# Performance work log

Hardware: AMD Instinct MI355X
Metric: run time of the kernel (lower is better)

The kernel has to match this reference:

```python
import jax, jax.numpy as jnp
import numpy as np


def setup_inputs() -> dict:
    key = jax.random.key(0)
    k1, = jax.random.split(key, 1)
    B, H, W, C = 16, 64, 64, 256
    x = jax.random.normal(k1, (B, H, W, C), dtype=jnp.float32)
    gamma = jnp.zeros((1,), dtype=jnp.float32)
    return {"x": x, "gamma": gamma}


def reference(x, gamma):
    B, H, W, C = x.shape
    a = x.reshape(B, H * W, C)                      # [B, HW, C]
    # aTa[b, i, j] = sum_n a[b, n, i] * a[b, n, j]  -> [B, C, C]
    aTa = jnp.einsum('bni,bnj->bij', a, a)
    attn = jax.nn.softmax(aTa, axis=-1)             # softmax over last channel axis
    # aaTa[b, n, j] = sum_i a[b, n, i] * attn[b, i, j]
    aaTa = jnp.einsum('bni,bij->bnj', a, attn)      # [B, HW, C]
    aaTa = aaTa.reshape(B, H, W, C)
    return gamma * aaTa + x
```

## Files before the change

### kernel.cpp

```cpp
#include <hip/hip_runtime.h>
#include <hip/hip_bf16.h>


#define BB 16
#define NN 4096
#define CC 256
#define SPLITK 8
#define KCHUNK (NN / SPLITK)

typedef __attribute__((ext_vector_type(4))) short short4v;
typedef __attribute__((ext_vector_type(8))) short short8v;
typedef __attribute__((ext_vector_type(4))) float floatx4;

__device__ __forceinline__ unsigned short f2bf(float f) {
    unsigned int u = __float_as_uint(f);
    u += 0x7fffu + ((u >> 16) & 1u);
    return (unsigned short)(u >> 16);
}
__device__ __forceinline__ short4v cvt4(floatx4 v) {
    short4v r;
    r[0] = (short)f2bf(v[0]); r[1] = (short)f2bf(v[1]);
    r[2] = (short)f2bf(v[2]); r[3] = (short)f2bf(v[3]);
    return r;
}

__global__ __launch_bounds__(512, 2) void k_gemm1(const float* __restrict__ x,
                                                  float* __restrict__ part) {
    __shared__ unsigned short P[2][256 * 72];
    const int split = blockIdx.x;
    const int b     = blockIdx.y;
    const int half  = blockIdx.z;
    const int t  = threadIdx.x;
    const int w  = t >> 6, l = t & 63;
    const int lk = (l >> 4) * 8;
    const int lm = l & 15;
    const int i0 = half * 128;
    const int wr = (w >> 2) * 64;
    const int wc = (w & 3) * 64;
    const unsigned swz = (unsigned)(l & 7) << 3;

    const float* xb = x + ((size_t)b * NN + (size_t)split * KCHUNK) * CC + 4 * l;

    floatx4 acc[4][4] = {};
    floatx4 pf[8];

    auto LOAD = [&](int k0) {
        const float* xn = xb + (size_t)k0 * CC;
        #pragma unroll
        for (int p = 0; p < 8; ++p)
            pf[p] = *(const floatx4*)(xn + (size_t)(w + 8 * p) * CC);
    };
    auto CVTWRITE = [&](unsigned short* Pd) {
        short4v s[8];
        #pragma unroll
        for (int p = 0; p < 8; ++p) s[p] = cvt4(pf[p]);
        #pragma unroll
        for (int j = 0; j < 4; ++j) {
            short8v o;
            #pragma unroll
            for (int e = 0; e < 8; ++e) o[e] = s[e][j];
            const unsigned c = (unsigned)(4 * l + j);
            *(short8v*)&Pd[c * 72 + (((unsigned)(8 * w)) ^ swz)] = o;
        }
    };
    auto MFMASTEP = [&](const unsigned short* Ps) {
        #pragma unroll
        for (int ks = 0; ks < 64; ks += 32) {
            short8v af[4], bf[4];
            #pragma unroll
            for (int mt = 0; mt < 4; ++mt) {
                const unsigned row = (unsigned)(i0 + wr + mt * 16 + lm);
                af[mt] = *(const short8v*)&Ps[row * 72 + (((unsigned)(ks + lk)) ^ (((row >> 2) & 7u) << 3))];
            }
            #pragma unroll
            for (int nt = 0; nt < 4; ++nt) {
                const unsigned row = (unsigned)(wc + nt * 16 + lm);
                bf[nt] = *(const short8v*)&Ps[row * 72 + (((unsigned)(ks + lk)) ^ (((row >> 2) & 7u) << 3))];
            }
            #pragma unroll
            for (int mt = 0; mt < 4; ++mt)
                #pragma unroll
                for (int nt = 0; nt < 4; ++nt)
                    acc[mt][nt] = __builtin_amdgcn_mfma_f32_16x16x32_bf16(af[mt], bf[nt], acc[mt][nt], 0, 0, 0);
        }
    };

    LOAD(0);
    CVTWRITE(P[0]);
    __syncthreads();

    #pragma unroll
    for (int s8 = 0; s8 < 8; ++s8) {
        if (s8 < 7) LOAD(s8 * 64 + 64);
        MFMASTEP(P[s8 & 1]);
        if (s8 < 7) CVTWRITE(P[(s8 & 1) ^ 1]);
        __syncthreads();
    }

    const int orow = (l >> 4) * 4;
    float* pout = part + (size_t)(split * BB + b) * CC * CC;
    #pragma unroll
    for (int mt = 0; mt < 4; ++mt)
        #pragma unroll
        for (int nt = 0; nt < 4; ++nt)
            #pragma unroll
            for (int r = 0; r < 4; ++r) {
                int i = i0 + wr + mt * 16 + orow + r;
                int j = wc + nt * 16 + lm;
                pout[(size_t)i * CC + j] = acc[mt][nt][r];
            }
}

__global__ __launch_bounds__(256) void k_softmax(const float* __restrict__ part,
                                                 unsigned short* __restrict__ attnT) {
    const int w = threadIdx.x >> 6;
    const int l = threadIdx.x & 63;
    const int row = blockIdx.x * 4 + w;
    const int b = row >> 8;
    const int i = row & 255;
    float v0 = 0.f, v1 = 0.f, v2 = 0.f, v3 = 0.f;
    #pragma unroll
    for (int s = 0; s < SPLITK; ++s) {
        const float* p = part + ((size_t)(s * BB + b) * CC + i) * CC;
        v0 += p[l]; v1 += p[l + 64]; v2 += p[l + 128]; v3 += p[l + 192];
    }
    float m = fmaxf(fmaxf(v0, v1), fmaxf(v2, v3));
    for (int off = 32; off >= 1; off >>= 1) m = fmaxf(m, __shfl_xor(m, off, 64));
    v0 = __expf(v0 - m); v1 = __expf(v1 - m); v2 = __expf(v2 - m); v3 = __expf(v3 - m);
    float s = v0 + v1 + v2 + v3;
    for (int off = 32; off >= 1; off >>= 1) s += __shfl_xor(s, off, 64);
    float rs = 1.0f / s;
    unsigned short* o = attnT + (size_t)b * CC * CC + i;
    o[(size_t)(l +   0) * CC] = f2bf(v0 * rs);
    o[(size_t)(l +  64) * CC] = f2bf(v1 * rs);
    o[(size_t)(l + 128) * CC] = f2bf(v2 * rs);
    o[(size_t)(l + 192) * CC] = f2bf(v3 * rs);
}

#define ALD 260
__global__ __launch_bounds__(256, 4) void k_gemm2(const float* __restrict__ x,
                                                  const unsigned short* __restrict__ attnT,
                                                  const float* __restrict__ gamma,
                                                  float* __restrict__ out) {
    __shared__ unsigned short At[64 * ALD];
    const int n0 = blockIdx.x * 64;
    const int b  = blockIdx.y;
    const int t  = threadIdx.x;
    const int w  = t >> 6, l = t & 63;
    const int lk = (l >> 4) * 8, lm = l & 15;

    const float* Abase = x + ((size_t)b * NN + n0) * CC;

    #pragma unroll
    for (int r = 0; r < 16; ++r) {
        int idx = r * 256 + t;
        int row = idx >> 6;
        int col = (idx & 63) * 4;
        floatx4 v = *(const floatx4*)(Abase + (size_t)row * CC + col);
        *(short4v*)&At[row * ALD + col] = cvt4(v);
    }
    __syncthreads();

    const unsigned short* Bb = attnT + (size_t)b * CC * CC;
    floatx4 acc[4][4] = {};
    #pragma unroll
    for (int k0 = 0; k0 < CC; k0 += 32) {
        short8v af[4], bf[4];
        #pragma unroll
        for (int mt = 0; mt < 4; ++mt)
            af[mt] = *(const short8v*)&At[(mt * 16 + lm) * ALD + k0 + lk];
        #pragma unroll
        for (int nt = 0; nt < 4; ++nt)
            bf[nt] = *(const short8v*)(Bb + (size_t)(w * 64 + nt * 16 + lm) * CC + k0 + lk);
        #pragma unroll
        for (int mt = 0; mt < 4; ++mt)
            #pragma unroll
            for (int nt = 0; nt < 4; ++nt)
                acc[mt][nt] = __builtin_amdgcn_mfma_f32_16x16x32_bf16(af[mt], bf[nt], acc[mt][nt], 0, 0, 0);
    }

    const float g = gamma[0];
    const int orow = (l >> 4) * 4;
    #pragma unroll
    for (int mt = 0; mt < 4; ++mt)
        #pragma unroll
        for (int nt = 0; nt < 4; ++nt) {
            float v0 = acc[mt][nt][0], v1 = acc[mt][nt][1];
            float v2 = acc[mt][nt][2], v3 = acc[mt][nt][3];
            float tt;
            tt = __shfl_xor((lm & 1) ? v0 : v1, 1, 64); if (lm & 1) v0 = tt; else v1 = tt;
            tt = __shfl_xor((lm & 1) ? v2 : v3, 1, 64); if (lm & 1) v2 = tt; else v3 = tt;
            tt = __shfl_xor((lm & 2) ? v0 : v2, 2, 64); if (lm & 2) v0 = tt; else v2 = tt;
            tt = __shfl_xor((lm & 2) ? v1 : v3, 2, 64); if (lm & 2) v1 = tt; else v3 = tt;
            int nr = n0 + mt * 16 + orow + (lm & 3);
            int jc = w * 64 + nt * 16 + (lm & 12);
            size_t ro = ((size_t)b * NN + nr) * CC + jc;
            floatx4 xv = *(const floatx4*)(x + ro);
            floatx4 ov;
            ov[0] = g * v0 + xv[0]; ov[1] = g * v1 + xv[1];
            ov[2] = g * v2 + xv[2]; ov[3] = g * v3 + xv[3];
            *(floatx4*)(out + ro) = ov;
        }
}

extern "C" void kernel_launch(void* const* d_in, const int* in_sizes, int n_in,
                              void* d_out, int out_size, void* d_ws, size_t ws_size,
                              hipStream_t stream) {
    const float* x     = (const float*)d_in[0];
    const float* gamma = (const float*)d_in[1];
    float* out = (float*)d_out;

    char* ws = (char*)d_ws;
    float*          part  = (float*)ws;
    unsigned short* attnT = (unsigned short*)(ws + (size_t)SPLITK * BB * CC * CC * 4);

    k_gemm1  <<<dim3(SPLITK, BB, 2),  512, 0, stream>>>(x, part);
    k_softmax<<<dim3(BB * CC / 4),    256, 0, stream>>>(part, attnT);
    k_gemm2  <<<dim3(NN / 64, BB),    256, 0, stream>>>(x, attnT, gamma, out);
}
```

Before: 159.7 us.

## Pipeline gemm2 over K chunks with double-buffered LDS tiles for A and B

Rewrites the second GEMM so that it no longer loads the full 64x256 activation tile into LDS up front and reads attention directly from global memory. It now steps through K in chunks of 32, prefetching both A (converted to bf16) and the attention tile into registers, then writing them into double-buffered LDS with a padded stride. The aim is to overlap global loads with MFMA work and to serve the B operand from LDS. In exchange the kernel does more synchronisation, the occupancy hint drops from 4 to 3, B staging gains no reuse across waves, and the 34-element stride makes 16-byte LDS accesses misaligned.

Measured after the change: 166.7 us. +4.4%, slower.

```diff
diff --git a/kernel.cpp b/kernel.cpp
--- a/kernel.cpp
+++ b/kernel.cpp
@@ -137,46 +137,70 @@
     o[(size_t)(l + 192) * CC] = f2bf(v3 * rs);
 }
 
-#define ALD 260
-__global__ __launch_bounds__(256, 4) void k_gemm2(const float* __restrict__ x,
+#define TLD 34
+__global__ __launch_bounds__(256, 3) void k_gemm2(const float* __restrict__ x,
                                                   const unsigned short* __restrict__ attnT,
                                                   const float* __restrict__ gamma,
                                                   float* __restrict__ out) {
-    __shared__ unsigned short At[64 * ALD];
+    __shared__ unsigned short At[2][64 * TLD];
+    __shared__ unsigned short Bt[2][256 * TLD];
     const int n0 = blockIdx.x * 64;
     const int b  = blockIdx.y;
     const int t  = threadIdx.x;
     const int w  = t >> 6, l = t & 63;
     const int lk = (l >> 4) * 8, lm = l & 15;
 
-    const float* Abase = x + ((size_t)b * NN + n0) * CC;
-
-    #pragma unroll
-    for (int r = 0; r < 16; ++r) {
-        int idx = r * 256 + t;
-        int row = idx >> 6;
-        int col = (idx & 63) * 4;
-        floatx4 v = *(const floatx4*)(Abase + (size_t)row * CC + col);
-        *(short4v*)&At[row * ALD + col] = cvt4(v);
-    }
-    __syncthreads();
-
+    const float*          Ab = x + ((size_t)b * NN + n0) * CC;
     const unsigned short* Bb = attnT + (size_t)b * CC * CC;
+
+    const int arow0 = t >> 3,      ach = (t & 7) * 4;
+    const int brow0 = t >> 2,      bch = (t & 3) * 8;
+
+    floatx4 pA0, pA1;
+    short8v pB0, pB1, pB2, pB3;
+
+    auto LOADT = [&](int k0) {
+        pA0 = *(const floatx4*)(Ab + (size_t)arow0 * CC + k0 + ach);
+        pA1 = *(const floatx4*)(Ab + (size_t)(arow0 + 32) * CC + k0 + ach);
+        pB0 = *(const short8v*)(Bb + (size_t)brow0 * CC + k0 + bch);
+        pB1 = *(const short8v*)(Bb + (size_t)(brow0 +  64) * CC + k0 + bch);
+        pB2 = *(const short8v*)(Bb + (size_t)(brow0 + 128) * CC + k0 + bch);
+        pB3 = *(const short8v*)(Bb + (size_t)(brow0 + 192) * CC + k0 + bch);
+    };
+    auto WRITET = [&](int buf) {
+        *(short4v*)&At[buf][arow0 * TLD + ach]        = cvt4(pA0);
+        *(short4v*)&At[buf][(arow0 + 32) * TLD + ach] = cvt4(pA1);
+        *(short8v*)&Bt[buf][brow0 * TLD + bch]         = pB0;
+        *(short8v*)&Bt[buf][(brow0 +  64) * TLD + bch] = pB1;
+        *(short8v*)&Bt[buf][(brow0 + 128) * TLD + bch] = pB2;
+        *(short8v*)&Bt[buf][(brow0 + 192) * TLD + bch] = pB3;
+    };
+
     floatx4 acc[4][4] = {};
-    #pragma unroll
-    for (int k0 = 0; k0 < CC; k0 += 32) {
+    auto MFMAT = [&](int buf) {
         short8v af[4], bf[4];
         #pragma unroll
         for (int mt = 0; mt < 4; ++mt)
-            af[mt] = *(const short8v*)&At[(mt * 16 + lm) * ALD + k0 + lk];
+            af[mt] = *(const short8v*)&At[buf][(mt * 16 + lm) * TLD + lk];
         #pragma unroll
         for (int nt = 0; nt < 4; ++nt)
-            bf[nt] = *(const short8v*)(Bb + (size_t)(w * 64 + nt * 16 + lm) * CC + k0 + lk);
+            bf[nt] = *(const short8v*)&Bt[buf][(w * 64 + nt * 16 + lm) * TLD + lk];
         #pragma unroll
         for (int mt = 0; mt < 4; ++mt)
             #pragma unroll
             for (int nt = 0; nt < 4; ++nt)
                 acc[mt][nt] = __builtin_amdgcn_mfma_f32_16x16x32_bf16(af[mt], bf[nt], acc[mt][nt], 0, 0, 0);
+    };
+
+    LOADT(0);
+    WRITET(0);
+    __syncthreads();
+    #pragma unroll
+    for (int s8 = 0; s8 < 8; ++s8) {
+        if (s8 < 7) LOADT(s8 * 32 + 32);
+        MFMAT(s8 & 1);
+        if (s8 < 7) WRITET((s8 & 1) ^ 1);
+        __syncthreads();
     }
 
     const float g = gamma[0];
```
